# Performance work log

Measured on AMD Instinct MI355X. Metric: run time of the kernel, lower is better.

## Reference

```python
import jax, jax.numpy as jnp
import numpy as np

NUM_ITER = 6  # matches init kwarg num_iter
N = 8388608


def setup_inputs() -> dict:
    key = jax.random.key(0)
    k1, k2 = jax.random.split(key, 2)
    # ray origins on plane x = -30, lateral extent inside the 50mm aperture
    yz = jax.random.uniform(k1, (N, 2), jnp.float32, -22.0, 22.0)
    P = jnp.concatenate([jnp.full((N, 1), -30.0, jnp.float32), yz], axis=1)
    # nearly-paraxial directions along +x, normalized
    dv = 0.05 * jax.random.normal(k2, (N, 2), jnp.float32)
    V = jnp.concatenate([jnp.ones((N, 1), jnp.float32), dv], axis=1)
    V = V / jnp.linalg.norm(V, axis=1, keepdims=True)
    tf_in = jnp.eye(4, dtype=jnp.float32)
    return {
        'P': P, 'V': V, 'tf_in': tf_in,
        'diameter': jnp.asarray(50.0, jnp.float32),
        'C': jnp.asarray(0.02, jnp.float32),
        'anchors': jnp.zeros((2,), jnp.float32),
        'scale': jnp.asarray(1.0, jnp.float32),
    }


def _translate_x(dx, dtype):
    return jnp.eye(4, dtype=dtype).at[0, 3].set(dx)


def reference(P, V, tf_in, diameter, C, anchors, scale):
    dtype = P.dtype

    def sag(y, z):
        # spherical sag: s(r) = C r^2 / (1 + sqrt(1 - C^2 r^2)); ds/dy = y*C/sqrt(.), ds/dz = z*C/sqrt(.)
        r2 = y * y + z * z
        sq = jnp.sqrt(jnp.clip(1.0 - C * C * r2, 1e-12))
        return C * r2 / (1.0 + sq), C / sq

    zero = jnp.zeros((), dtype)
    ext0, _ = sag(anchors[0] * diameter * 0.5, zero)
    ext1, _ = sag(anchors[1] * diameter * 0.5, zero)

    one = jnp.ones((), dtype)
    S = jnp.diag(jnp.stack([scale, scale, scale, one]))
    tf_surface = tf_in @ _translate_x(-scale * ext0, dtype) @ S
    tf_next = tf_in @ _translate_x(scale * (ext1 - ext0), dtype)

    M = tf_surface[:3, :3]
    b = tf_surface[:3, 3]
    Minv = jnp.linalg.inv(M)
    Pl = (P - b) @ Minv.T   # rays in local surface frame
    Vl = V @ Minv.T

    def F_grad(t):
        Q = Pl + t[:, None] * Vl           # [N,3] current iterate
        sv, d = sag(Q[:, 1], Q[:, 2])
        F = sv - Q[:, 0]                   # implicit residual: sag(y,z) - x
        g = jnp.stack([-jnp.ones_like(F), d * Q[:, 1], d * Q[:, 2]], axis=1)
        return Q, F, g

    def step(t, _):
        _, F, g = F_grad(t)
        denom = jnp.sum(g * Vl, axis=1)
        denom = jnp.where(jnp.abs(denom) > 1e-12, denom, 1e-12)
        return t - F / denom, None

    t0 = jnp.zeros(P.shape[0], dtype)
    t, _ = jax.lax.scan(step, t0, None, length=NUM_ITER)

    Q, F, g = F_grad(t)
    r2 = Q[:, 1] ** 2 + Q[:, 2] ** 2
    valid = (r2 <= (diameter * 0.5) ** 2) & (jnp.abs(F) < 1e-3) & (C * C * r2 < 1.0)

    nl = g / jnp.linalg.norm(g, axis=1, keepdims=True)
    n = nl @ Minv                          # normals transform by M^{-T}
    n = n / jnp.linalg.norm(n, axis=1, keepdims=True)
    return t, n, valid, tf_surface, tf_next
```

## Files before the change

### kernel.cpp

```cpp
#include <hip/hip_runtime.h>
#include <math.h>

__global__ void setup_k(const float* __restrict__ tf_in,
                        const float* __restrict__ diameter,
                        const float* __restrict__ C,
                        const float* __restrict__ anchors,
                        const float* __restrict__ scale,
                        float* __restrict__ tf_out,
                        float* __restrict__ ws) {
    float Cv = C[0], dia = diameter[0], sc = scale[0];
    float a0 = anchors[0] * dia * 0.5f;
    float a1 = anchors[1] * dia * 0.5f;
    float r20 = a0 * a0, r21 = a1 * a1;
    float sq0 = sqrtf(fmaxf(1.0f - Cv * Cv * r20, 1e-12f));
    float sq1 = sqrtf(fmaxf(1.0f - Cv * Cv * r21, 1e-12f));
    float ext0 = Cv * r20 / (1.0f + sq0);
    float ext1 = Cv * r21 / (1.0f + sq1);
    float dx0 = -sc * ext0;
    float dx1 = sc * (ext1 - ext0);

    float M[9], b[3];
    for (int r = 0; r < 4; ++r) {
        float t0 = tf_in[r*4+0], t1 = tf_in[r*4+1], t2 = tf_in[r*4+2], t3 = tf_in[r*4+3];
        tf_out[r*4+0] = t0 * sc;
        tf_out[r*4+1] = t1 * sc;
        tf_out[r*4+2] = t2 * sc;
        tf_out[r*4+3] = t0 * dx0 + t3;
        tf_out[16 + r*4+0] = t0;
        tf_out[16 + r*4+1] = t1;
        tf_out[16 + r*4+2] = t2;
        tf_out[16 + r*4+3] = t0 * dx1 + t3;
        if (r < 3) {
            M[r*3+0] = t0 * sc; M[r*3+1] = t1 * sc; M[r*3+2] = t2 * sc;
            b[r] = t0 * dx0 + t3;
        }
    }
    float c00 =  (M[4]*M[8] - M[5]*M[7]);
    float c01 = -(M[3]*M[8] - M[5]*M[6]);
    float c02 =  (M[3]*M[7] - M[4]*M[6]);
    float det = M[0]*c00 + M[1]*c01 + M[2]*c02;
    float id = 1.0f / det;
    float inv[9];
    inv[0] =  c00 * id;
    inv[1] = -(M[1]*M[8] - M[2]*M[7]) * id;
    inv[2] =  (M[1]*M[5] - M[2]*M[4]) * id;
    inv[3] =  c01 * id;
    inv[4] =  (M[0]*M[8] - M[2]*M[6]) * id;
    inv[5] = -(M[0]*M[5] - M[2]*M[3]) * id;
    inv[6] =  c02 * id;
    inv[7] = -(M[0]*M[7] - M[1]*M[6]) * id;
    inv[8] =  (M[0]*M[4] - M[1]*M[3]) * id;
    #pragma unroll
    for (int i = 0; i < 9; ++i) ws[i] = inv[i];
    ws[9]  = b[0]; ws[10] = b[1]; ws[11] = b[2];
    ws[12] = Cv;
    ws[13] = (dia * 0.5f) * (dia * 0.5f);
    ws[14] = Cv * Cv;
    ws[15] = 1.0f / Cv;
}

__device__ __forceinline__ float frcp(float x) { return __builtin_amdgcn_rcpf(x); }
__device__ __forceinline__ float frsq(float x) { return __builtin_amdgcn_rsqf(x); }

struct v4 { float a, b, c, d; };
__device__ __forceinline__ v4 vadd(v4 x, v4 y) { return {x.a+y.a, x.b+y.b, x.c+y.c, x.d+y.d}; }
__device__ __forceinline__ v4 vsub(v4 x, v4 y) { return {x.a-y.a, x.b-y.b, x.c-y.c, x.d-y.d}; }
__device__ __forceinline__ v4 vmul(v4 x, v4 y) { return {x.a*y.a, x.b*y.b, x.c*y.c, x.d*y.d}; }
__device__ __forceinline__ v4 vmuls(v4 x, float s) { return {x.a*s, x.b*s, x.c*s, x.d*s}; }
__device__ __forceinline__ v4 vfma(v4 x, v4 y, v4 z) {
    return {fmaf(x.a,y.a,z.a), fmaf(x.b,y.b,z.b), fmaf(x.c,y.c,z.c), fmaf(x.d,y.d,z.d)};
}
__device__ __forceinline__ v4 vfmas(v4 x, float s, v4 z) {
    return {fmaf(x.a,s,z.a), fmaf(x.b,s,z.b), fmaf(x.c,s,z.c), fmaf(x.d,s,z.d)};
}
__device__ __forceinline__ v4 vmaxs(v4 x, float s) {
    return {fmaxf(x.a,s), fmaxf(x.b,s), fmaxf(x.c,s), fmaxf(x.d,s)};
}
__device__ __forceinline__ v4 vrsq(v4 x) { return {frsq(x.a), frsq(x.b), frsq(x.c), frsq(x.d)}; }
__device__ __forceinline__ v4 vrcp(v4 x) { return {frcp(x.a), frcp(x.b), frcp(x.c), frcp(x.d)}; }
__device__ __forceinline__ v4 vneg(v4 x) { return {-x.a, -x.b, -x.c, -x.d}; }
__device__ __forceinline__ float clampden(float x) { return (fabsf(x) > 1e-12f) ? x : 1e-12f; }
__device__ __forceinline__ v4 vclampden(v4 x) {
    return {clampden(x.a), clampden(x.b), clampden(x.c), clampden(x.d)};
}

__global__ __launch_bounds__(256) void trace_k(
    const float4* __restrict__ P4, const float4* __restrict__ V4,
    const float* __restrict__ ws,
    float4* __restrict__ t_out4, float4* __restrict__ n_out4,
    float4* __restrict__ valid_out4, int ngroups) {
    int g = blockIdx.x * blockDim.x + threadIdx.x;
    if (g >= ngroups) return;

    const float m00 = ws[0], m01 = ws[1], m02 = ws[2];
    const float m10 = ws[3], m11 = ws[4], m12 = ws[5];
    const float m20 = ws[6], m21 = ws[7], m22 = ws[8];
    const float b0 = ws[9], b1 = ws[10], b2 = ws[11];
    const float Cv = ws[12], rmax2 = ws[13], cc = ws[14], invC = ws[15];

    float4 pA = P4[(size_t)g*3+0], pB = P4[(size_t)g*3+1], pC = P4[(size_t)g*3+2];
    float4 vA = V4[(size_t)g*3+0], vB = V4[(size_t)g*3+1], vC = V4[(size_t)g*3+2];

    v4 px = {pA.x, pA.w, pB.z, pC.y};
    v4 py = {pA.y, pB.x, pB.w, pC.z};
    v4 pz = {pA.z, pB.y, pC.x, pC.w};
    v4 vx = {vA.x, vA.w, vB.z, vC.y};
    v4 vy = {vA.y, vB.x, vB.w, vC.z};
    v4 vz = {vA.z, vB.y, vC.x, vC.w};

    v4 nb0 = {-b0,-b0,-b0,-b0}, nb1 = {-b1,-b1,-b1,-b1}, nb2 = {-b2,-b2,-b2,-b2};
    v4 dpx = vadd(px, nb0), dpy = vadd(py, nb1), dpz = vadd(pz, nb2);
    v4 Pl0 = vfmas(dpx, m00, vfmas(dpy, m01, vmuls(dpz, m02)));
    v4 Pl1 = vfmas(dpx, m10, vfmas(dpy, m11, vmuls(dpz, m12)));
    v4 Pl2 = vfmas(dpx, m20, vfmas(dpy, m21, vmuls(dpz, m22)));
    v4 Vl0 = vfmas(vx, m00, vfmas(vy, m01, vmuls(vz, m02)));
    v4 Vl1 = vfmas(vx, m10, vfmas(vy, m11, vmuls(vz, m12)));
    v4 Vl2 = vfmas(vx, m20, vfmas(vy, m21, vmuls(vz, m22)));

    const v4 one = {1.0f, 1.0f, 1.0f, 1.0f};
    v4 t = {0.0f, 0.0f, 0.0f, 0.0f};

    #pragma unroll
    for (int it = 0; it < 6; ++it) {
        v4 q1 = vfma(t, Vl1, Pl1);
        v4 q2 = vfma(t, Vl2, Pl2);
        v4 r2 = vfma(q1, q1, vmul(q2, q2));
        v4 w  = vmaxs(vfmas(r2, -cc, one), 1e-12f);
        v4 rs = vrsq(w);
        v4 sq = vmul(w, rs);
        v4 d  = vmuls(rs, Cv);
        v4 sv = vfmas(sq, -invC, {invC, invC, invC, invC});
        v4 q0 = vfma(t, Vl0, Pl0);
        v4 F  = vsub(sv, q0);
        v4 dot = vfma(q2, Vl2, vmul(q1, Vl1));
        v4 denom = vclampden(vfma(d, dot, vneg(Vl0)));
        t = vfma(vneg(F), vrcp(denom), t);
    }

    v4 q0 = vfma(t, Vl0, Pl0);
    v4 q1 = vfma(t, Vl1, Pl1);
    v4 q2 = vfma(t, Vl2, Pl2);
    v4 r2 = vfma(q1, q1, vmul(q2, q2));
    v4 wp = vfmas(r2, -cc, one);
    v4 w  = vmaxs(wp, 1e-12f);
    v4 rs = vrsq(w);
    v4 sq = vmul(w, rs);
    v4 d  = vmuls(rs, Cv);
    v4 sv = vfmas(sq, -invC, {invC, invC, invC, invC});
    v4 F  = vsub(sv, q0);

    v4 g1 = vmul(d, q1), g2 = vmul(d, q2);
    v4 nm00 = {-m00,-m00,-m00,-m00}, nm01 = {-m01,-m01,-m01,-m01}, nm02 = {-m02,-m02,-m02,-m02};
    v4 n0 = vfmas(g1, m10, vfmas(g2, m20, nm00));
    v4 n1 = vfmas(g1, m11, vfmas(g2, m21, nm01));
    v4 n2 = vfmas(g1, m12, vfmas(g2, m22, nm02));
    v4 ninv = vrsq(vfma(n0, n0, vfma(n1, n1, vmul(n2, n2))));
    n0 = vmul(n0, ninv); n1 = vmul(n1, ninv); n2 = vmul(n2, ninv);

    float vda = (r2.a <= rmax2 && fabsf(F.a) < 0.001f && wp.a > 0.0f) ? 1.0f : 0.0f;
    float vdb = (r2.b <= rmax2 && fabsf(F.b) < 0.001f && wp.b > 0.0f) ? 1.0f : 0.0f;
    float vdc = (r2.c <= rmax2 && fabsf(F.c) < 0.001f && wp.c > 0.0f) ? 1.0f : 0.0f;
    float vdd = (r2.d <= rmax2 && fabsf(F.d) < 0.001f && wp.d > 0.0f) ? 1.0f : 0.0f;

    t_out4[g]     = make_float4(t.a, t.b, t.c, t.d);
    valid_out4[g] = make_float4(vda, vdb, vdc, vdd);
    n_out4[(size_t)g*3+0] = make_float4(n0.a, n1.a, n2.a, n0.b);
    n_out4[(size_t)g*3+1] = make_float4(n1.b, n2.b, n0.c, n1.c);
    n_out4[(size_t)g*3+2] = make_float4(n2.c, n0.d, n1.d, n2.d);
}

__global__ void trace_tail_k(const float* __restrict__ P, const float* __restrict__ V,
                             const float* __restrict__ ws,
                             float* __restrict__ t_out, float* __restrict__ n_out,
                             float* __restrict__ valid_out, int start, int N) {
    int i = start + blockIdx.x * blockDim.x + threadIdx.x;
    if (i >= N) return;
    const float m00 = ws[0], m01 = ws[1], m02 = ws[2];
    const float m10 = ws[3], m11 = ws[4], m12 = ws[5];
    const float m20 = ws[6], m21 = ws[7], m22 = ws[8];
    const float b0 = ws[9], b1 = ws[10], b2 = ws[11];
    const float Cv = ws[12], rmax2 = ws[13], cc = ws[14], invC = ws[15];
    float dpx = P[i*3+0] - b0, dpy = P[i*3+1] - b1, dpz = P[i*3+2] - b2;
    float Pl0 = m00*dpx + m01*dpy + m02*dpz;
    float Pl1 = m10*dpx + m11*dpy + m12*dpz;
    float Pl2 = m20*dpx + m21*dpy + m22*dpz;
    float Vl0 = m00*V[i*3+0] + m01*V[i*3+1] + m02*V[i*3+2];
    float Vl1 = m10*V[i*3+0] + m11*V[i*3+1] + m12*V[i*3+2];
    float Vl2 = m20*V[i*3+0] + m21*V[i*3+1] + m22*V[i*3+2];
    float t = 0.0f;
    for (int it = 0; it < 6; ++it) {
        float q1 = Pl1 + t*Vl1, q2 = Pl2 + t*Vl2;
        float r2 = q1*q1 + q2*q2;
        float w  = fmaxf(1.0f - cc*r2, 1e-12f);
        float rs = frsq(w);
        float sq = w * rs;
        float d  = Cv * rs;
        float sv = fmaf(sq, -invC, invC);
        float F  = sv - (Pl0 + t*Vl0);
        float denom = d*(q1*Vl1 + q2*Vl2) - Vl0;
        denom = (fabsf(denom) > 1e-12f) ? denom : 1e-12f;
        t = t - F * frcp(denom);
    }
    float q0 = Pl0 + t*Vl0, q1 = Pl1 + t*Vl1, q2 = Pl2 + t*Vl2;
    float r2 = q1*q1 + q2*q2;
    float wp = 1.0f - cc*r2;
    float w  = fmaxf(wp, 1e-12f);
    float rs = frsq(w);
    float sq = w * rs;
    float d  = Cv * rs;
    float sv = fmaf(sq, -invC, invC);
    float F  = sv - q0;
    bool valid = (r2 <= rmax2) && (fabsf(F) < 0.001f) && (wp > 0.0f);
    float g1 = d*q1, g2 = d*q2;
    float n0 = -m00 + g1*m10 + g2*m20;
    float n1 = -m01 + g1*m11 + g2*m21;
    float n2 = -m02 + g1*m12 + g2*m22;
    float ninv = frsq(n0*n0 + n1*n1 + n2*n2);
    t_out[i] = t;
    n_out[i*3+0] = n0*ninv; n_out[i*3+1] = n1*ninv; n_out[i*3+2] = n2*ninv;
    valid_out[i] = valid ? 1.0f : 0.0f;
}

extern "C" void kernel_launch(void* const* d_in, const int* in_sizes, int n_in,
                              void* d_out, int out_size, void* d_ws, size_t ws_size,
                              hipStream_t stream) {
    const float* P       = (const float*)d_in[0];
    const float* V       = (const float*)d_in[1];
    const float* tf_in   = (const float*)d_in[2];
    const float* dia     = (const float*)d_in[3];
    const float* C       = (const float*)d_in[4];
    const float* anchors = (const float*)d_in[5];
    const float* scale   = (const float*)d_in[6];
    const int N = in_sizes[0] / 3;

    float* out = (float*)d_out;
    float* ws  = (float*)d_ws;

    float* t_out     = out;
    float* n_out     = out + (size_t)N;
    float* valid_out = out + (size_t)4*N;
    float* tf_out    = out + (size_t)5*N;

    setup_k<<<1, 1, 0, stream>>>(tf_in, dia, C, anchors, scale, tf_out, ws);

    const int ngroups = N / 4;
    const int block = 256;
    const int grid = (ngroups + block - 1) / block;
    trace_k<<<grid, block, 0, stream>>>((const float4*)P, (const float4*)V, ws,
                                        (float4*)t_out, (float4*)n_out,
                                        (float4*)valid_out, ngroups);
    const int rem = N - ngroups * 4;
    if (rem > 0) {
        trace_tail_k<<<1, 64, 0, stream>>>(P, V, ws, t_out, n_out, valid_out,
                                           ngroups * 4, N);
    }
}
```

Baseline: 78.39 us.

## Stage ray loads and normal stores through shared memory for coalesced access

Each block now handles a tile of 1024 rays. It loads P and V as fully coalesced float4 rows into LDS, transposes them there so each thread gets four strided rays, and writes normals back through LDS the same way. t and valid become scalar stores coalesced across threads. The goal is to replace the three strided float4 accesses per thread with contiguous wavefront accesses, at the cost of 24KB LDS per block, extra barriers, and possible LDS bank conflicts from the stride-3 indexing.

New measurement: 77.59 us. No clear change (-1.0%).

```diff
diff --git a/kernel.cpp b/kernel.cpp
--- a/kernel.cpp
+++ b/kernel.cpp
@@ -87,10 +87,31 @@
 __global__ __launch_bounds__(256) void trace_k(
     const float4* __restrict__ P4, const float4* __restrict__ V4,
     const float* __restrict__ ws,
-    float4* __restrict__ t_out4, float4* __restrict__ n_out4,
-    float4* __restrict__ valid_out4, int ngroups) {
-    int g = blockIdx.x * blockDim.x + threadIdx.x;
-    if (g >= ngroups) return;
+    float* __restrict__ t_out, float4* __restrict__ n_out4,
+    float* __restrict__ valid_out, int ntiles) {
+    __shared__ float sP[3072];
+    __shared__ float sV[3072];
+    const int tid = threadIdx.x;
+    const int blk = blockIdx.x;
+    if (blk >= ntiles) return;
+
+    const size_t fbase = (size_t)blk * 768;
+
+    float4 pr0 = P4[fbase + 0*256 + tid];
+    float4 pr1 = P4[fbase + 1*256 + tid];
+    float4 pr2 = P4[fbase + 2*256 + tid];
+    float4 vr0 = V4[fbase + 0*256 + tid];
+    float4 vr1 = V4[fbase + 1*256 + tid];
+    float4 vr2 = V4[fbase + 2*256 + tid];
+    float4* sP4 = (float4*)sP;
+    float4* sV4 = (float4*)sV;
+    sP4[0*256 + tid] = pr0;
+    sP4[1*256 + tid] = pr1;
+    sP4[2*256 + tid] = pr2;
+    sV4[0*256 + tid] = vr0;
+    sV4[1*256 + tid] = vr1;
+    sV4[2*256 + tid] = vr2;
+    __syncthreads();
 
     const float m00 = ws[0], m01 = ws[1], m02 = ws[2];
     const float m10 = ws[3], m11 = ws[4], m12 = ws[5];
@@ -98,24 +119,29 @@
     const float b0 = ws[9], b1 = ws[10], b2 = ws[11];
     const float Cv = ws[12], rmax2 = ws[13], cc = ws[14], invC = ws[15];
 
-    float4 pA = P4[(size_t)g*3+0], pB = P4[(size_t)g*3+1], pC = P4[(size_t)g*3+2];
-    float4 vA = V4[(size_t)g*3+0], vB = V4[(size_t)g*3+1], vC = V4[(size_t)g*3+2];
-
-    v4 px = {pA.x, pA.w, pB.z, pC.y};
-    v4 py = {pA.y, pB.x, pB.w, pC.z};
-    v4 pz = {pA.z, pB.y, pC.x, pC.w};
-    v4 vx = {vA.x, vA.w, vB.z, vC.y};
-    v4 vy = {vA.y, vB.x, vB.w, vC.z};
-    v4 vz = {vA.z, vB.y, vC.x, vC.w};
-
-    v4 nb0 = {-b0,-b0,-b0,-b0}, nb1 = {-b1,-b1,-b1,-b1}, nb2 = {-b2,-b2,-b2,-b2};
-    v4 dpx = vadd(px, nb0), dpy = vadd(py, nb1), dpz = vadd(pz, nb2);
-    v4 Pl0 = vfmas(dpx, m00, vfmas(dpy, m01, vmuls(dpz, m02)));
-    v4 Pl1 = vfmas(dpx, m10, vfmas(dpy, m11, vmuls(dpz, m12)));
-    v4 Pl2 = vfmas(dpx, m20, vfmas(dpy, m21, vmuls(dpz, m22)));
-    v4 Vl0 = vfmas(vx, m00, vfmas(vy, m01, vmuls(vz, m02)));
-    v4 Vl1 = vfmas(vx, m10, vfmas(vy, m11, vmuls(vz, m12)));
-    v4 Vl2 = vfmas(vx, m20, vfmas(vy, m21, vmuls(vz, m22)));
+    float Pl0a[4], Pl1a[4], Pl2a[4], Vl0a[4], Vl1a[4], Vl2a[4];
+    #pragma unroll
+    for (int k = 0; k < 4; ++k) {
+        const int el = k*256 + tid;
+        float dpx = sP[el*3+0] - b0;
+        float dpy = sP[el*3+1] - b1;
+        float dpz = sP[el*3+2] - b2;
+        float wx  = sV[el*3+0], wy = sV[el*3+1], wz = sV[el*3+2];
+        Pl0a[k] = fmaf(dpx, m00, fmaf(dpy, m01, dpz*m02));
+        Pl1a[k] = fmaf(dpx, m10, fmaf(dpy, m11, dpz*m12));
+        Pl2a[k] = fmaf(dpx, m20, fmaf(dpy, m21, dpz*m22));
+        Vl0a[k] = fmaf(wx, m00, fmaf(wy, m01, wz*m02));
+        Vl1a[k] = fmaf(wx, m10, fmaf(wy, m11, wz*m12));
+        Vl2a[k] = fmaf(wx, m20, fmaf(wy, m21, wz*m22));
+    }
+    __syncthreads();
+
+    v4 Pl0 = {Pl0a[0], Pl0a[1], Pl0a[2], Pl0a[3]};
+    v4 Pl1 = {Pl1a[0], Pl1a[1], Pl1a[2], Pl1a[3]};
+    v4 Pl2 = {Pl2a[0], Pl2a[1], Pl2a[2], Pl2a[3]};
+    v4 Vl0 = {Vl0a[0], Vl0a[1], Vl0a[2], Vl0a[3]};
+    v4 Vl1 = {Vl1a[0], Vl1a[1], Vl1a[2], Vl1a[3]};
+    v4 Vl2 = {Vl2a[0], Vl2a[1], Vl2a[2], Vl2a[3]};
 
     const v4 one = {1.0f, 1.0f, 1.0f, 1.0f};
     v4 t = {0.0f, 0.0f, 0.0f, 0.0f};
@@ -157,16 +183,30 @@
     v4 ninv = vrsq(vfma(n0, n0, vfma(n1, n1, vmul(n2, n2))));
     n0 = vmul(n0, ninv); n1 = vmul(n1, ninv); n2 = vmul(n2, ninv);
 
-    float vda = (r2.a <= rmax2 && fabsf(F.a) < 0.001f && wp.a > 0.0f) ? 1.0f : 0.0f;
-    float vdb = (r2.b <= rmax2 && fabsf(F.b) < 0.001f && wp.b > 0.0f) ? 1.0f : 0.0f;
-    float vdc = (r2.c <= rmax2 && fabsf(F.c) < 0.001f && wp.c > 0.0f) ? 1.0f : 0.0f;
-    float vdd = (r2.d <= rmax2 && fabsf(F.d) < 0.001f && wp.d > 0.0f) ? 1.0f : 0.0f;
-
-    t_out4[g]     = make_float4(t.a, t.b, t.c, t.d);
-    valid_out4[g] = make_float4(vda, vdb, vdc, vdd);
-    n_out4[(size_t)g*3+0] = make_float4(n0.a, n1.a, n2.a, n0.b);
-    n_out4[(size_t)g*3+1] = make_float4(n1.b, n2.b, n0.c, n1.c);
-    n_out4[(size_t)g*3+2] = make_float4(n2.c, n0.d, n1.d, n2.d);
+    float ta[4]  = {t.a, t.b, t.c, t.d};
+    float n0a[4] = {n0.a, n0.b, n0.c, n0.d};
+    float n1a[4] = {n1.a, n1.b, n1.c, n1.d};
+    float n2a[4] = {n2.a, n2.b, n2.c, n2.d};
+    float r2a[4] = {r2.a, r2.b, r2.c, r2.d};
+    float Fa[4]  = {F.a, F.b, F.c, F.d};
+    float wpa[4] = {wp.a, wp.b, wp.c, wp.d};
+
+    const size_t ebase = (size_t)blk * 1024;
+    #pragma unroll
+    for (int k = 0; k < 4; ++k) {
+        const int el = k*256 + tid;
+        sP[el*3+0] = n0a[k];
+        sP[el*3+1] = n1a[k];
+        sP[el*3+2] = n2a[k];
+        t_out[ebase + el] = ta[k];
+        valid_out[ebase + el] =
+            (r2a[k] <= rmax2 && fabsf(Fa[k]) < 0.001f && wpa[k] > 0.0f) ? 1.0f : 0.0f;
+    }
+    __syncthreads();
+
+    n_out4[fbase + 0*256 + tid] = sP4[0*256 + tid];
+    n_out4[fbase + 1*256 + tid] = sP4[1*256 + tid];
+    n_out4[fbase + 2*256 + tid] = sP4[2*256 + tid];
 }
 
 __global__ void trace_tail_k(const float* __restrict__ P, const float* __restrict__ V,
@@ -243,15 +283,15 @@
 
     setup_k<<<1, 1, 0, stream>>>(tf_in, dia, C, anchors, scale, tf_out, ws);
 
-    const int ngroups = N / 4;
-    const int block = 256;
-    const int grid = (ngroups + block - 1) / block;
-    trace_k<<<grid, block, 0, stream>>>((const float4*)P, (const float4*)V, ws,
-                                        (float4*)t_out, (float4*)n_out,
-                                        (float4*)valid_out, ngroups);
-    const int rem = N - ngroups * 4;
+    const int ntiles = N / 1024;
+    if (ntiles > 0) {
+        trace_k<<<ntiles, 256, 0, stream>>>((const float4*)P, (const float4*)V, ws,
+                                            t_out, (float4*)n_out, valid_out, ntiles);
+    }
+    const int start = ntiles * 1024;
+    const int rem = N - start;
     if (rem > 0) {
-        trace_tail_k<<<1, 64, 0, stream>>>(P, V, ws, t_out, n_out, valid_out,
-                                           ngroups * 4, N);
-    }
-}
+        trace_tail_k<<<(rem + 255) / 256, 256, 0, stream>>>(P, V, ws, t_out, n_out,
+                                                            valid_out, start, N);
+    }
+}
```
